# Performance work log

Measured on AMD Instinct MI355X. Metric: run time of the kernel, lower is better.

The kernel has to match this reference:

```python
import jax, jax.numpy as jnp
import numpy as np

VOCAB_SIZE = 62  # string.ascii_letters + string.digits
HIDDEN = 1024
STATE = int(HIDDEN * 4.0)  # state_size_mult=4.0
B, L = 2, 2048


def setup_inputs() -> dict:
    key = jax.random.key(0)
    ks = jax.random.split(key, 6)
    g = lambda k, shape, scale: (jax.random.normal(k, shape, jnp.float32) * scale)
    return {
        "tokens": jax.random.randint(ks[0], (B, L), 0, VOCAB_SIZE),
        "embed_w": g(ks[1], (VOCAB_SIZE, HIDDEN), 1.0),
        "norm_w": jnp.ones((HIDDEN,), jnp.float32),
        "in_w": g(ks[2], (HIDDEN, 4 * STATE), HIDDEN ** -0.5),
        "in_b": jnp.zeros((4 * STATE,), jnp.float32),
        "out_w": g(ks[3], (STATE, HIDDEN), STATE ** -0.5),
        "out_b": jnp.zeros((HIDDEN,), jnp.float32),
        "head_w": g(ks[4], (HIDDEN, VOCAB_SIZE), HIDDEN ** -0.5),
        "head_b": jnp.zeros((VOCAB_SIZE,), jnp.float32),
    }


def _rmsnorm(x, w, eps=1e-6):
    var = jnp.mean(x * x, axis=-1, keepdims=True)
    return x * jax.lax.rsqrt(var + eps) * w


def reference(tokens, embed_w, norm_w, in_w, in_b, out_w, out_b, head_w, head_b):
    # embedding lookup: [B, L, H]
    x = embed_w[tokens]
    res = x
    xn = _rmsnorm(x, norm_w)
    # single fused projection to (x_inner, a, b, c), each [B, L, STATE]
    proj = xn @ in_w + in_b
    xg, a_l, b_l, c_l = jnp.split(proj, 4, axis=-1)
    a = jax.nn.sigmoid(a_l)            # forget gate in (0,1)
    bx = jax.nn.sigmoid(b_l) * xg      # input contribution b_t * x_t
    # linear recurrence h_t = a_t * h_{t-1} + b_t * x_t via associative scan
    def comb(e1, e2):
        a1, h1 = e1
        a2, h2 = e2
        return a1 * a2, a2 * h1 + h2
    _, h = jax.lax.associative_scan(comb, (a, bx), axis=1)
    y = jax.nn.sigmoid(c_l) * h        # output gate c_t * h_t
    out = y @ out_w + out_b + res      # project back to hidden + residual
    return out @ head_w + head_b       # vocab logits [B, L, 62]
```

## Files before the change

### kernel.cpp

```cpp
#include <hip/hip_runtime.h>
#include <math.h>

#define HID   1024
#define STT   4096
#define MTOK  4096
#define LSEQ  2048
#define NCHUNK 64
#define CHUNK  32
#define VOCAB  62

typedef __attribute__((ext_vector_type(8))) short short8v;
typedef __attribute__((ext_vector_type(4))) float float4v;

typedef const __attribute__((address_space(1))) void* gptr_t;
typedef __attribute__((address_space(3))) void* lptr_t;

__device__ __forceinline__ float sigmoidf_(float x) {
    return 1.0f / (1.0f + __expf(-x));
}
__device__ __forceinline__ unsigned short f2bf(float f) {
    unsigned int u = __float_as_uint(f);
    unsigned int r = (u + 0x7fffu + ((u >> 16) & 1u)) >> 16;
    return (unsigned short)r;
}
__device__ __forceinline__ float bf2f(unsigned short b) {
    return __uint_as_float(((unsigned int)b) << 16);
}

__global__ __launch_bounds__(256) void fused_pre(
    const int* __restrict__ tokens, const float* __restrict__ embed_w,
    const float* __restrict__ norm_w, const float* __restrict__ in_w,
    const float* __restrict__ out_w, const float* __restrict__ head_w,
    const float* __restrict__ out_b, const float* __restrict__ head_b,
    unsigned short* __restrict__ in_wT, unsigned short* __restrict__ xn,
    unsigned short* __restrict__ W2T, float* __restrict__ E_head)
{
    __shared__ float sh[1056];
    int bid = blockIdx.x;
    int tid = threadIdx.x;
    if (bid < 16384) {
        float (*tile)[33] = (float (*)[33])sh;
        int c0 = (bid & 511) * 32, r0 = (bid >> 9) * 32;
        int r = tid >> 3, c4 = (tid & 7) << 2;
        float4 v = *(const float4*)(in_w + (size_t)(r0 + r) * 16384 + c0 + c4);
        tile[r][c4 + 0] = v.x; tile[r][c4 + 1] = v.y;
        tile[r][c4 + 2] = v.z; tile[r][c4 + 3] = v.w;
        __syncthreads();
        int oc = tid >> 3;
        int orr = (tid & 7) << 2;
        ushort4 o;
        o.x = f2bf(tile[orr + 0][oc]); o.y = f2bf(tile[orr + 1][oc]);
        o.z = f2bf(tile[orr + 2][oc]); o.w = f2bf(tile[orr + 3][oc]);
        *(ushort4*)(in_wT + (size_t)(c0 + oc) * 1024 + r0 + orr) = o;
    } else if (bid < 20480) {
        int m = bid - 16384;
        int tok = tokens[m];
        float4 x = ((const float4*)(embed_w + (size_t)tok * HID))[tid];
        float ss = x.x * x.x + x.y * x.y + x.z * x.z + x.w * x.w;
        for (int off = 32; off > 0; off >>= 1) ss += __shfl_down(ss, off);
        if ((tid & 63) == 0) sh[tid >> 6] = ss;
        __syncthreads();
        float tot = sh[0] + sh[1] + sh[2] + sh[3];
        float scale = rsqrtf(tot / (float)HID + 1e-6f);
        float4 w4 = ((const float4*)norm_w)[tid];
        ushort4 o;
        o.x = f2bf(x.x * scale * w4.x); o.y = f2bf(x.y * scale * w4.y);
        o.z = f2bf(x.z * scale * w4.z); o.w = f2bf(x.w * scale * w4.w);
        *(ushort4*)(xn + (size_t)m * HID + (tid << 2)) = o;
    } else if (bid < 21504) {
        float (*red)[4][64] = (float (*)[4][64])sh;
        int jc = tid >> 6, n = tid & 63;
        bool act = n < VOCAB;
        int k0 = (bid - 20480) * 4;
        float a[4] = {0.f, 0.f, 0.f, 0.f};
        int j0 = jc * 256;
        const float* w0 = out_w + (size_t)(k0 + 0) * HID;
        const float* w1 = out_w + (size_t)(k0 + 1) * HID;
        const float* w2 = out_w + (size_t)(k0 + 2) * HID;
        const float* w3 = out_w + (size_t)(k0 + 3) * HID;
        #pragma unroll 4
        for (int j = j0; j < j0 + 256; j++) {
            float h = act ? head_w[(size_t)j * VOCAB + n] : 0.f;
            a[0] = fmaf(w0[j], h, a[0]);
            a[1] = fmaf(w1[j], h, a[1]);
            a[2] = fmaf(w2[j], h, a[2]);
            a[3] = fmaf(w3[j], h, a[3]);
        }
        #pragma unroll
        for (int i = 0; i < 4; i++) red[jc][i][n] = a[i];
        __syncthreads();
        if (jc == 0) {
            #pragma unroll
            for (int i = 0; i < 4; i++) {
                float s = red[0][i][n] + red[1][i][n] + red[2][i][n] + red[3][i][n];
                W2T[(size_t)n * STT + k0 + i] = f2bf(s);
            }
        }
    } else {
        float (*red)[4][64] = (float (*)[4][64])sh;
        int jc = tid >> 6, n = tid & 63;
        bool act = n < VOCAB;
        int t = bid - 21504;
        const float* src = (t < VOCAB) ? (embed_w + (size_t)t * HID) : out_b;
        float acc = 0.f;
        if (act) {
            int j0 = jc * 256;
            #pragma unroll 4
            for (int j = j0; j < j0 + 256; j++)
                acc = fmaf(src[j], head_w[(size_t)j * VOCAB + n], acc);
        }
        red[jc][0][n] = acc;
        __syncthreads();
        if (tid < 64) {
            float s = red[0][0][n] + red[1][0][n] + red[2][0][n] + red[3][0][n];
            if (t == VOCAB && act) s += head_b[n];
            E_head[t * 64 + n] = s;
        }
    }
}

__global__ __launch_bounds__(512, 2) void gemm_in_mfma(
    const unsigned short* __restrict__ A, const unsigned short* __restrict__ B,
    const float* __restrict__ bias,
    unsigned short* __restrict__ a_out, unsigned short* __restrict__ bx_out,
    unsigned short* __restrict__ c_out,
    float* __restrict__ chunkA, float* __restrict__ chunkH)
{
    extern __shared__ unsigned short lds[];
    int tid = threadIdx.x;
    int wid = tid >> 6, lane = tid & 63;
    int wg = blockIdx.x;
    int xcd = wg & 7, loc = wg >> 3;
    int by = ((xcd >> 1) << 2) + (loc & 3);
    int bx = ((xcd & 1) << 5) + (loc >> 2);
    int m0 = by * 256, s0 = bx * 64;
    int wm = wid >> 2, wn = wid & 3;
    int lr = lane & 15, lk = lane >> 4;

    int cb0 = wid * 64, cb1 = 512 + wid * 64;
    int p0 = cb0 + lane, p1 = cb1 + lane;
    int row0 = p0 >> 2, ks0 = (p0 & 3) ^ ((row0 >> 1) & 3);
    int row1 = p1 >> 2, ks1 = (p1 & 3) ^ ((row1 >> 1) & 3);
    int arow0 = m0 + row0, arow1 = m0 + row1;
    int brow0 = ((row0 >> 6) << 12) + s0 + (row0 & 63);
    int brow1 = ((row1 >> 6) << 12) + s0 + (row1 & 63);

#define SHALF(grow0, grow1, b, which, kt, kk) do {                               \
    unsigned short* _d = lds + (b) * 32768 + (which) * 16384 + (kk) * 8192;      \
    __builtin_amdgcn_global_load_lds(                                            \
        (gptr_t)(const void*)(((which) ? B : A) + (size_t)(grow0) * 1024 +       \
                              (kt) * 64 + (kk) * 32 + ks0 * 8),                  \
        (lptr_t)(void*)(_d + (size_t)cb0 * 8), 16, 0, 0);                        \
    __builtin_amdgcn_global_load_lds(                                            \
        (gptr_t)(const void*)(((which) ? B : A) + (size_t)(grow1) * 1024 +       \
                              (kt) * 64 + (kk) * 32 + ks1 * 8),                  \
        (lptr_t)(void*)(_d + (size_t)cb1 * 8), 16, 0, 0);                        \
} while (0)

    int ksw = lk ^ ((lr >> 1) & 3);

#define RD_A(b, kk, mf) \
    (*(const short8v*)&lds[(b) * 32768 + (kk) * 8192 + \
        (((wm * 128 + (mf) * 16 + lr) << 2) + ksw) * 8])
#define RD_B(b, kk, nf) \
    (*(const short8v*)&lds[(b) * 32768 + 16384 + (kk) * 8192 + \
        ((((nf) * 64 + wn * 16 + lr) << 2) + ksw) * 8])

#define MFMA8x2(AF, B0, B1, n0i, n1i) do {                                       \
    __builtin_amdgcn_s_setprio(1);                                               \
    _Pragma("unroll")                                                            \
    for (int mf = 0; mf < 8; mf++) {                                             \
        acc[mf][n0i] = __builtin_amdgcn_mfma_f32_16x16x32_bf16(                  \
            (AF)[mf], (B0), acc[mf][n0i], 0, 0, 0);                              \
        acc[mf][n1i] = __builtin_amdgcn_mfma_f32_16x16x32_bf16(                  \
            (AF)[mf], (B1), acc[mf][n1i], 0, 0, 0);                              \
    }                                                                            \
    __builtin_amdgcn_s_setprio(0);                                               \
} while (0)

#define BAR_IN()  do { __builtin_amdgcn_s_barrier();                              \
    asm volatile("s_waitcnt lgkmcnt(0)" ::: "memory");                           \
    __builtin_amdgcn_sched_barrier(0); } while (0)
#define BAR_OUT() do { asm volatile("" ::: "memory");                             \
    __builtin_amdgcn_s_barrier(); } while (0)

    float4v acc[8][4];
    float4v z = {0.f, 0.f, 0.f, 0.f};
    #pragma unroll
    for (int i = 0; i < 8; i++)
        #pragma unroll
        for (int j = 0; j < 4; j++) acc[i][j] = z;

    SHALF(arow0, arow1, 0, 0, 0, 0); SHALF(brow0, brow1, 0, 1, 0, 0);
    SHALF(arow0, arow1, 0, 0, 0, 1); SHALF(brow0, brow1, 0, 1, 0, 1);
    asm volatile("s_waitcnt vmcnt(0)" ::: "memory");
    __builtin_amdgcn_s_barrier();

    short8v af[8], bf0, bf1;

    for (int kt = 0; kt < 16; ++kt) {
        int cur = kt & 1, nxt = cur ^ 1;
        int ktn = kt < 15 ? kt + 1 : 15;
        #pragma unroll
        for (int mf = 0; mf < 8; mf++) af[mf] = RD_A(cur, 0, mf);
        bf0 = RD_B(cur, 0, 0); bf1 = RD_B(cur, 0, 1);
        asm volatile("s_waitcnt vmcnt(4)" ::: "memory");
        SHALF(arow0, arow1, nxt, 0, ktn, 0);
        BAR_IN();
        MFMA8x2(af, bf0, bf1, 0, 1);
        BAR_OUT();
        bf0 = RD_B(cur, 0, 2); bf1 = RD_B(cur, 0, 3);
        SHALF(brow0, brow1, nxt, 1, ktn, 0);
        BAR_IN();
        MFMA8x2(af, bf0, bf1, 2, 3);
        BAR_OUT();
        #pragma unroll
        for (int mf = 0; mf < 8; mf++) af[mf] = RD_A(cur, 1, mf);
        bf0 = RD_B(cur, 1, 0); bf1 = RD_B(cur, 1, 1);
        asm volatile("s_waitcnt vmcnt(4)" ::: "memory");
        SHALF(arow0, arow1, nxt, 0, ktn, 1);
        BAR_IN();
        MFMA8x2(af, bf0, bf1, 0, 1);
        BAR_OUT();
        bf0 = RD_B(cur, 1, 2); bf1 = RD_B(cur, 1, 3);
        SHALF(brow0, brow1, nxt, 1, ktn, 1);
        BAR_IN();
        MFMA8x2(af, bf0, bf1, 2, 3);
        BAR_OUT();
    }

    int s = s0 + wn * 16 + lr;
    float b_xg = bias[s];
    float b_a  = bias[4096 + s];
    float b_b  = bias[8192 + s];
    float b_c  = bias[12288 + s];
    int rbase = lk << 2;
    int bb = m0 >> 11;
    int t0 = m0 & 2047;
    int ch = bb * STT + s;

    #pragma unroll
    for (int cc = 0; cc < 4; cc++) {
        float Afr[2], Hfr[2];
        #pragma unroll
        for (int e = 0; e < 2; e++) {
            int mf = cc * 2 + e;
            float Al = 1.f, Hl = 0.f;
            #pragma unroll
            for (int q = 0; q < 4; q++) {
                int m = m0 + wm * 128 + mf * 16 + rbase + q;
                size_t idx = (size_t)m * STT + s;
                float xg = acc[mf][0][q] + b_xg;
                float av = sigmoidf_(acc[mf][1][q] + b_a);
                float bxv = sigmoidf_(acc[mf][2][q] + b_b) * xg;
                float cv = sigmoidf_(acc[mf][3][q] + b_c);
                unsigned short au = f2bf(av), bu = f2bf(bxv);
                a_out[idx]  = au;
                bx_out[idx] = bu;
                c_out[idx]  = f2bf(cv);
                float ar = bf2f(au), br = bf2f(bu);
                Hl = fmaf(ar, Hl, br);
                Al = ar * Al;
            }
            #pragma unroll
            for (int d = 1; d <= 2; d <<= 1) {
                float Ap = __shfl(Al, lane - (d << 4));
                float Hp = __shfl(Hl, lane - (d << 4));
                if (lk >= d) { Hl = fmaf(Al, Hp, Hl); Al = Al * Ap; }
            }
            Afr[e] = Al; Hfr[e] = Hl;
        }
        if (lk == 3) {
            float Ac = Afr[1] * Afr[0];
            float Hc = fmaf(Afr[1], Hfr[0], Hfr[1]);
            int qg = (t0 >> 5) + wm * 4 + cc;
            chunkA[ch * NCHUNK + qg] = Ac;
            chunkH[ch * NCHUNK + qg] = Hc;
        }
    }
#undef SHALF
#undef RD_A
#undef RD_B
#undef MFMA8x2
#undef BAR_IN
#undef BAR_OUT
}

__global__ __launch_bounds__(256) void scan_phase2(
    const float* __restrict__ chunkA, const float* __restrict__ chunkH,
    float* __restrict__ carry)
{
    int ch = blockIdx.x * 256 + threadIdx.x;
    float c = 0.f;
    for (int q = 0; q < NCHUNK; q++) {
        carry[ch * NCHUNK + q] = c;
        c = fmaf(chunkA[ch * NCHUNK + q], c, chunkH[ch * NCHUNK + q]);
    }
}

__global__ __launch_bounds__(256) void scan_logits(
    const unsigned short* __restrict__ a_buf, const unsigned short* __restrict__ bx_buf,
    const unsigned short* __restrict__ c_buf, const float* __restrict__ carry,
    const unsigned short* __restrict__ W2T, float* __restrict__ part)
{
    __shared__ __align__(16) unsigned short y_lds[128 * 128];
    __shared__ __align__(16) unsigned short b_lds[64 * 128];
    int tid = threadIdx.x;
    int wg = blockIdx.x;
    int mt = wg & 31, sl = wg >> 5;
    int m0 = mt * 128;
    int bb = m0 >> 11;
    int q0 = (m0 & 2047) >> 5;
    int lane = tid & 63, wid = tid >> 6;
    int lr = lane & 15, lk = lane >> 4;

    float4v acc[2][4];
    float4v z = {0.f, 0.f, 0.f, 0.f};
    #pragma unroll
    for (int e = 0; e < 2; e++)
        #pragma unroll
        for (int nf = 0; nf < 4; nf++) acc[e][nf] = z;

    for (int ks = 0; ks < 4; ++ks) {
        int sbase = sl * 512 + ks * 128;
        #pragma unroll
        for (int i = 0; i < 4; i++) {
            int cb = i * 256 + wid * 64;
            int p = cb + lane;
            int row = p >> 4, csw = p & 15;
            int c = csw ^ (row & 7);
            __builtin_amdgcn_global_load_lds(
                (gptr_t)(const void*)(W2T + (size_t)row * STT + sbase + c * 8),
                (lptr_t)(void*)(b_lds + (size_t)cb * 8), 16, 0, 0);
        }
        {
            int chq = wid;
            int s = sbase + lane * 2;
            int q = q0 + chq;
            size_t cidx = ((size_t)(bb * STT + s)) * NCHUNK + q;
            float h0 = carry[cidx];
            float h1 = carry[cidx + NCHUNK];
            size_t gb = (size_t)(m0 + chq * 32) * STT + s;
            const unsigned int* ap = (const unsigned int*)(a_buf + gb);
            const unsigned int* bp = (const unsigned int*)(bx_buf + gb);
            const unsigned int* cp = (const unsigned int*)(c_buf + gb);
            const int stride = STT / 2;
            #pragma unroll 4
            for (int i = 0; i < 32; i++) {
                unsigned int au = ap[(size_t)i * stride];
                unsigned int bu = bp[(size_t)i * stride];
                unsigned int cu = cp[(size_t)i * stride];
                float a0 = bf2f((unsigned short)(au & 0xffff));
                float a1 = bf2f((unsigned short)(au >> 16));
                float b0 = bf2f((unsigned short)(bu & 0xffff));
                float b1 = bf2f((unsigned short)(bu >> 16));
                float c0 = bf2f((unsigned short)(cu & 0xffff));
                float c1 = bf2f((unsigned short)(cu >> 16));
                h0 = fmaf(a0, h0, b0);
                h1 = fmaf(a1, h1, b1);
                unsigned int yp = (unsigned int)f2bf(c0 * h0) |
                                  ((unsigned int)f2bf(c1 * h1) << 16);
                int row = chq * 32 + i;
                int cw = (lane >> 2) ^ (row & 7);
                *(unsigned int*)&y_lds[row * 128 + (cw << 3) + (lane & 3) * 2] = yp;
            }
        }
        __syncthreads();
        #pragma unroll
        for (int kt2 = 0; kt2 < 4; kt2++) {
            short8v af[2], bf[4];
            #pragma unroll
            for (int e = 0; e < 2; e++) {
                int row = (wid * 2 + e) * 16 + lr;
                int c = kt2 * 4 + lk;
                af[e] = *(const short8v*)&y_lds[row * 128 + ((c ^ (row & 7)) << 3)];
            }
            #pragma unroll
            for (int nf = 0; nf < 4; nf++) {
                int row = nf * 16 + lr;
                int c = kt2 * 4 + lk;
                bf[nf] = *(const short8v*)&b_lds[row * 128 + ((c ^ (row & 7)) << 3)];
            }
            __builtin_amdgcn_s_setprio(1);
            #pragma unroll
            for (int e = 0; e < 2; e++)
                #pragma unroll
                for (int nf = 0; nf < 4; nf++)
                    acc[e][nf] = __builtin_amdgcn_mfma_f32_16x16x32_bf16(
                        af[e], bf[nf], acc[e][nf], 0, 0, 0);
            __builtin_amdgcn_s_setprio(0);
        }
        __syncthreads();
    }

    float* pb = part + (size_t)sl * MTOK * 64;
    int rbase = lk << 2;
    #pragma unroll
    for (int e = 0; e < 2; e++)
        #pragma unroll
        for (int nf = 0; nf < 4; nf++) {
            int n = nf * 16 + lr;
            #pragma unroll
            for (int q = 0; q < 4; q++) {
                int m = m0 + (wid * 2 + e) * 16 + rbase + q;
                pb[(size_t)m * 64 + n] = acc[e][nf][q];
            }
        }
}

__global__ __launch_bounds__(64) void logits_reduce(
    const float* __restrict__ part, const float* __restrict__ E_head,
    const int* __restrict__ tokens, float* __restrict__ logits)
{
    int m = blockIdx.x;
    int n = threadIdx.x;
    if (n >= VOCAB) return;
    int tok = tokens[m];
    float s = E_head[tok * 64 + n] + E_head[VOCAB * 64 + n];
    #pragma unroll
    for (int sl = 0; sl < 8; sl++)
        s += part[(size_t)sl * MTOK * 64 + (size_t)m * 64 + n];
    logits[(size_t)m * VOCAB + n] = s;
}

extern "C" void kernel_launch(void* const* d_in, const int* in_sizes, int n_in,
                              void* d_out, int out_size, void* d_ws, size_t ws_size,
                              hipStream_t stream) {
    const int*   tokens  = (const int*)d_in[0];
    const float* embed_w = (const float*)d_in[1];
    const float* norm_w  = (const float*)d_in[2];
    const float* in_w    = (const float*)d_in[3];
    const float* in_b    = (const float*)d_in[4];
    const float* out_w   = (const float*)d_in[5];
    const float* out_b   = (const float*)d_in[6];
    const float* head_w  = (const float*)d_in[7];
    const float* head_b  = (const float*)d_in[8];
    float* logits = (float*)d_out;

    char* w = (char*)d_ws;
    unsigned short* a_buf  = (unsigned short*)w;
    unsigned short* bx_buf = (unsigned short*)(w + 33554432);
    unsigned short* c_buf  = (unsigned short*)(w + 67108864);
    unsigned short* W2T    = (unsigned short*)(w + 100663296);
    float*          E_head = (float*)(w + 101711872);
    float*          part   = (float*)(w + 102760448);
    unsigned short* in_wT  = (unsigned short*)(w + 167772160);
    unsigned short* xn     = (unsigned short*)(w + 201326592);
    float* chunkA = (float*)(w + 209715200);
    float* chunkH = chunkA + 8192 * NCHUNK;
    float* carry  = chunkH + 8192 * NCHUNK;

    hipLaunchKernelGGL(fused_pre, dim3(16384 + 4096 + 1024 + VOCAB + 1), dim3(256), 0, stream,
                       tokens, embed_w, norm_w, in_w, out_w, head_w, out_b, head_b,
                       in_wT, xn, W2T, E_head);
    hipLaunchKernelGGL(gemm_in_mfma, dim3(1024), dim3(512), 131072, stream,
                       xn, in_wT, in_b, a_buf, bx_buf, c_buf, chunkA, chunkH);
    hipLaunchKernelGGL(scan_phase2, dim3(32), dim3(256), 0, stream,
                       chunkA, chunkH, carry);
    hipLaunchKernelGGL(scan_logits, dim3(256), dim3(256), 0, stream,
                       a_buf, bx_buf, c_buf, carry, W2T, part);
    hipLaunchKernelGGL(logits_reduce, dim3(MTOK), dim3(64), 0, stream,
                       part, E_head, tokens, logits);
}
```

Before: 265.2 us.

## Replace partial-sum buffer and reduce kernel with atomic logits accumulation

Removes the logits_reduce kernel and the partial buffer. A new scan2_init kernel runs the carry scan and also writes the bias/embedding-head base logits. scan_logits now splits the state dimension into 16 slices over 512 blocks and atomically adds its partial results straight into the logits. This saves a launch and the partial-buffer round trip, and doubles the scan_logits grid, at the cost of float atomics contention and non-deterministic summation order.

```diff
diff --git a/kernel.cpp b/kernel.cpp
--- a/kernel.cpp
+++ b/kernel.cpp
@@ -286,22 +286,35 @@
 #undef BAR_OUT
 }
 
-__global__ __launch_bounds__(256) void scan_phase2(
+__global__ __launch_bounds__(256) void scan2_init(
     const float* __restrict__ chunkA, const float* __restrict__ chunkH,
-    float* __restrict__ carry)
+    const float* __restrict__ E_head, const int* __restrict__ tokens,
+    float* __restrict__ carry, float* __restrict__ logits)
 {
-    int ch = blockIdx.x * 256 + threadIdx.x;
-    float c = 0.f;
-    for (int q = 0; q < NCHUNK; q++) {
-        carry[ch * NCHUNK + q] = c;
-        c = fmaf(chunkA[ch * NCHUNK + q], c, chunkH[ch * NCHUNK + q]);
+    int bid = blockIdx.x;
+    int tid = threadIdx.x;
+    if (bid < 32) {
+        int ch = bid * 256 + tid;
+        float c = 0.f;
+        for (int q = 0; q < NCHUNK; q++) {
+            carry[ch * NCHUNK + q] = c;
+            c = fmaf(chunkA[ch * NCHUNK + q], c, chunkH[ch * NCHUNK + q]);
+        }
+    } else {
+        int m = (bid - 32) * 4 + (tid >> 6);
+        int n = tid & 63;
+        if (n < VOCAB) {
+            int tok = tokens[m];
+            logits[(size_t)m * VOCAB + n] =
+                E_head[tok * 64 + n] + E_head[VOCAB * 64 + n];
+        }
     }
 }
 
 __global__ __launch_bounds__(256) void scan_logits(
     const unsigned short* __restrict__ a_buf, const unsigned short* __restrict__ bx_buf,
     const unsigned short* __restrict__ c_buf, const float* __restrict__ carry,
-    const unsigned short* __restrict__ W2T, float* __restrict__ part)
+    const unsigned short* __restrict__ W2T, float* __restrict__ logits)
 {
     __shared__ __align__(16) unsigned short y_lds[128 * 128];
     __shared__ __align__(16) unsigned short b_lds[64 * 128];
@@ -321,8 +334,8 @@
         #pragma unroll
         for (int nf = 0; nf < 4; nf++) acc[e][nf] = z;
 
-    for (int ks = 0; ks < 4; ++ks) {
-        int sbase = sl * 512 + ks * 128;
+    for (int ks = 0; ks < 2; ++ks) {
+        int sbase = sl * 256 + ks * 128;
         #pragma unroll
         for (int i = 0; i < 4; i++) {
             int cb = i * 256 + wid * 64;
@@ -393,34 +406,20 @@
         __syncthreads();
     }
 
-    float* pb = part + (size_t)sl * MTOK * 64;
     int rbase = lk << 2;
     #pragma unroll
     for (int e = 0; e < 2; e++)
         #pragma unroll
         for (int nf = 0; nf < 4; nf++) {
             int n = nf * 16 + lr;
-            #pragma unroll
-            for (int q = 0; q < 4; q++) {
-                int m = m0 + (wid * 2 + e) * 16 + rbase + q;
-                pb[(size_t)m * 64 + n] = acc[e][nf][q];
-            }
-        }
-}
-
-__global__ __launch_bounds__(64) void logits_reduce(
-    const float* __restrict__ part, const float* __restrict__ E_head,
-    const int* __restrict__ tokens, float* __restrict__ logits)
-{
-    int m = blockIdx.x;
-    int n = threadIdx.x;
-    if (n >= VOCAB) return;
-    int tok = tokens[m];
-    float s = E_head[tok * 64 + n] + E_head[VOCAB * 64 + n];
-    #pragma unroll
-    for (int sl = 0; sl < 8; sl++)
-        s += part[(size_t)sl * MTOK * 64 + (size_t)m * 64 + n];
-    logits[(size_t)m * VOCAB + n] = s;
+            if (n < VOCAB) {
+                #pragma unroll
+                for (int q = 0; q < 4; q++) {
+                    int m = m0 + (wid * 2 + e) * 16 + rbase + q;
+                    atomicAdd(&logits[(size_t)m * VOCAB + n], acc[e][nf][q]);
+                }
+            }
+        }
 }
 
 extern "C" void kernel_launch(void* const* d_in, const int* in_sizes, int n_in,
@@ -443,7 +442,6 @@
     unsigned short* c_buf  = (unsigned short*)(w + 67108864);
     unsigned short* W2T    = (unsigned short*)(w + 100663296);
     float*          E_head = (float*)(w + 101711872);
-    float*          part   = (float*)(w + 102760448);
     unsigned short* in_wT  = (unsigned short*)(w + 167772160);
     unsigned short* xn     = (unsigned short*)(w + 201326592);
     float* chunkA = (float*)(w + 209715200);
@@ -455,10 +453,8 @@
                        in_wT, xn, W2T, E_head);
     hipLaunchKernelGGL(gemm_in_mfma, dim3(1024), dim3(512), 131072, stream,
                        xn, in_wT, in_b, a_buf, bx_buf, c_buf, chunkA, chunkH);
-    hipLaunchKernelGGL(scan_phase2, dim3(32), dim3(256), 0, stream,
-                       chunkA, chunkH, carry);
-    hipLaunchKernelGGL(scan_logits, dim3(256), dim3(256), 0, stream,
-                       a_buf, bx_buf, c_buf, carry, W2T, part);
-    hipLaunchKernelGGL(logits_reduce, dim3(MTOK), dim3(64), 0, stream,
-                       part, E_head, tokens, logits);
-}
+    hipLaunchKernelGGL(scan2_init, dim3(32 + 1024), dim3(256), 0, stream,
+                       chunkA, chunkH, E_head, tokens, carry, logits);
+    hipLaunchKernelGGL(scan_logits, dim3(512), dim3(256), 0, stream,
+                       a_buf, bx_buf, c_buf, carry, W2T, logits);
+}
```

After: 277.4 us. 1.05x slower.

## Simplify input GEMM to K=32 double-buffered stages with single barrier pair

Applied to the files above, without the earlier changes.

Replaces the finely interleaved K=64 pipeline, which had four half-stage loads and barrier pairs per iteration, with a simple double-buffered loop over K=32 tiles. Each iteration issues one stage load, waits, runs a single barrier, and does all 32 MFMAs. LDS use halves from 128KB to 64KB, which could allow two workgroups per CU. The cost is that far less data is in flight per K step, so memory latency is hidden less well, and there are twice as many iterations, each with barrier overhead.

```diff
diff --git a/kernel.cpp b/kernel.cpp
--- a/kernel.cpp
+++ b/kernel.cpp
@@ -145,44 +145,31 @@
     int brow0 = ((row0 >> 6) << 12) + s0 + (row0 & 63);
     int brow1 = ((row1 >> 6) << 12) + s0 + (row1 & 63);
 
-#define SHALF(grow0, grow1, b, which, kt, kk) do {                               \
-    unsigned short* _d = lds + (b) * 32768 + (which) * 16384 + (kk) * 8192;      \
+#define STAGE(b, kt) do {                                                        \
+    unsigned short* _a = lds + (b) * 16384;                                      \
+    unsigned short* _b = _a + 8192;                                              \
     __builtin_amdgcn_global_load_lds(                                            \
-        (gptr_t)(const void*)(((which) ? B : A) + (size_t)(grow0) * 1024 +       \
-                              (kt) * 64 + (kk) * 32 + ks0 * 8),                  \
-        (lptr_t)(void*)(_d + (size_t)cb0 * 8), 16, 0, 0);                        \
+        (gptr_t)(const void*)(A + (size_t)arow0 * 1024 + (kt) * 32 + ks0 * 8),   \
+        (lptr_t)(void*)(_a + (size_t)cb0 * 8), 16, 0, 0);                        \
     __builtin_amdgcn_global_load_lds(                                            \
-        (gptr_t)(const void*)(((which) ? B : A) + (size_t)(grow1) * 1024 +       \
-                              (kt) * 64 + (kk) * 32 + ks1 * 8),                  \
-        (lptr_t)(void*)(_d + (size_t)cb1 * 8), 16, 0, 0);                        \
+        (gptr_t)(const void*)(A + (size_t)arow1 * 1024 + (kt) * 32 + ks1 * 8),   \
+        (lptr_t)(void*)(_a + (size_t)cb1 * 8), 16, 0, 0);                        \
+    __builtin_amdgcn_global_load_lds(                                            \
+        (gptr_t)(const void*)(B + (size_t)brow0 * 1024 + (kt) * 32 + ks0 * 8),   \
+        (lptr_t)(void*)(_b + (size_t)cb0 * 8), 16, 0, 0);                        \
+    __builtin_amdgcn_global_load_lds(                                            \
+        (gptr_t)(const void*)(B + (size_t)brow1 * 1024 + (kt) * 32 + ks1 * 8),   \
+        (lptr_t)(void*)(_b + (size_t)cb1 * 8), 16, 0, 0);                        \
 } while (0)
 
     int ksw = lk ^ ((lr >> 1) & 3);
 
-#define RD_A(b, kk, mf) \
-    (*(const short8v*)&lds[(b) * 32768 + (kk) * 8192 + \
+#define RD_A(b, mf) \
+    (*(const short8v*)&lds[(b) * 16384 + \
         (((wm * 128 + (mf) * 16 + lr) << 2) + ksw) * 8])
-#define RD_B(b, kk, nf) \
-    (*(const short8v*)&lds[(b) * 32768 + 16384 + (kk) * 8192 + \
+#define RD_B(b, nf) \
+    (*(const short8v*)&lds[(b) * 16384 + 8192 + \
         ((((nf) * 64 + wn * 16 + lr) << 2) + ksw) * 8])
-
-#define MFMA8x2(AF, B0, B1, n0i, n1i) do {                                       \
-    __builtin_amdgcn_s_setprio(1);                                               \
-    _Pragma("unroll")                                                            \
-    for (int mf = 0; mf < 8; mf++) {                                             \
-        acc[mf][n0i] = __builtin_amdgcn_mfma_f32_16x16x32_bf16(                  \
-            (AF)[mf], (B0), acc[mf][n0i], 0, 0, 0);                              \
-        acc[mf][n1i] = __builtin_amdgcn_mfma_f32_16x16x32_bf16(                  \
-            (AF)[mf], (B1), acc[mf][n1i], 0, 0, 0);                              \
-    }                                                                            \
-    __builtin_amdgcn_s_setprio(0);                                               \
-} while (0)
-
-#define BAR_IN()  do { __builtin_amdgcn_s_barrier();                              \
-    asm volatile("s_waitcnt lgkmcnt(0)" ::: "memory");                           \
-    __builtin_amdgcn_sched_barrier(0); } while (0)
-#define BAR_OUT() do { asm volatile("" ::: "memory");                             \
-    __builtin_amdgcn_s_barrier(); } while (0)
 
     float4v acc[8][4];
     float4v z = {0.f, 0.f, 0.f, 0.f};
@@ -191,42 +178,33 @@
         #pragma unroll
         for (int j = 0; j < 4; j++) acc[i][j] = z;
 
-    SHALF(arow0, arow1, 0, 0, 0, 0); SHALF(brow0, brow1, 0, 1, 0, 0);
-    SHALF(arow0, arow1, 0, 0, 0, 1); SHALF(brow0, brow1, 0, 1, 0, 1);
-    asm volatile("s_waitcnt vmcnt(0)" ::: "memory");
-    __builtin_amdgcn_s_barrier();
-
-    short8v af[8], bf0, bf1;
-
-    for (int kt = 0; kt < 16; ++kt) {
+    STAGE(0, 0);
+
+    for (int kt = 0; kt < 32; ++kt) {
         int cur = kt & 1, nxt = cur ^ 1;
-        int ktn = kt < 15 ? kt + 1 : 15;
-        #pragma unroll
-        for (int mf = 0; mf < 8; mf++) af[mf] = RD_A(cur, 0, mf);
-        bf0 = RD_B(cur, 0, 0); bf1 = RD_B(cur, 0, 1);
-        asm volatile("s_waitcnt vmcnt(4)" ::: "memory");
-        SHALF(arow0, arow1, nxt, 0, ktn, 0);
-        BAR_IN();
-        MFMA8x2(af, bf0, bf1, 0, 1);
-        BAR_OUT();
-        bf0 = RD_B(cur, 0, 2); bf1 = RD_B(cur, 0, 3);
-        SHALF(brow0, brow1, nxt, 1, ktn, 0);
-        BAR_IN();
-        MFMA8x2(af, bf0, bf1, 2, 3);
-        BAR_OUT();
-        #pragma unroll
-        for (int mf = 0; mf < 8; mf++) af[mf] = RD_A(cur, 1, mf);
-        bf0 = RD_B(cur, 1, 0); bf1 = RD_B(cur, 1, 1);
-        asm volatile("s_waitcnt vmcnt(4)" ::: "memory");
-        SHALF(arow0, arow1, nxt, 0, ktn, 1);
-        BAR_IN();
-        MFMA8x2(af, bf0, bf1, 0, 1);
-        BAR_OUT();
-        bf0 = RD_B(cur, 1, 2); bf1 = RD_B(cur, 1, 3);
-        SHALF(brow0, brow1, nxt, 1, ktn, 1);
-        BAR_IN();
-        MFMA8x2(af, bf0, bf1, 2, 3);
-        BAR_OUT();
+        if (kt < 31) {
+            STAGE(nxt, kt + 1);
+            asm volatile("s_waitcnt vmcnt(4)" ::: "memory");
+        } else {
+            asm volatile("s_waitcnt vmcnt(0)" ::: "memory");
+        }
+        __builtin_amdgcn_s_barrier();
+        asm volatile("" ::: "memory");
+        short8v af[8], bf[4];
+        #pragma unroll
+        for (int mf = 0; mf < 8; mf++) af[mf] = RD_A(cur, mf);
+        #pragma unroll
+        for (int nf = 0; nf < 4; nf++) bf[nf] = RD_B(cur, nf);
+        __builtin_amdgcn_s_setprio(1);
+        #pragma unroll
+        for (int mf = 0; mf < 8; mf++)
+            #pragma unroll
+            for (int nf = 0; nf < 4; nf++)
+                acc[mf][nf] = __builtin_amdgcn_mfma_f32_16x16x32_bf16(
+                    af[mf], bf[nf], acc[mf][nf], 0, 0, 0);
+        __builtin_amdgcn_s_setprio(0);
+        asm volatile("" ::: "memory");
+        __builtin_amdgcn_s_barrier();
     }
 
     int s = s0 + wn * 16 + lr;
@@ -278,12 +256,9 @@
             chunkH[ch * NCHUNK + qg] = Hc;
         }
     }
-#undef SHALF
+#undef STAGE
 #undef RD_A
 #undef RD_B
-#undef MFMA8x2
-#undef BAR_IN
-#undef BAR_OUT
 }
 
 __global__ __launch_bounds__(256) void scan_phase2(
@@ -453,7 +428,7 @@
     hipLaunchKernelGGL(fused_pre, dim3(16384 + 4096 + 1024 + VOCAB + 1), dim3(256), 0, stream,
                        tokens, embed_w, norm_w, in_w, out_w, head_w, out_b, head_b,
                        in_wT, xn, W2T, E_head);
-    hipLaunchKernelGGL(gemm_in_mfma, dim3(1024), dim3(512), 131072, stream,
+    hipLaunchKernelGGL(gemm_in_mfma, dim3(1024), dim3(512), 65536, stream,
                        xn, in_wT, in_b, a_buf, bx_buf, c_buf, chunkA, chunkH);
     hipLaunchKernelGGL(scan_phase2, dim3(32), dim3(256), 0, stream,
                        chunkA, chunkH, carry);
```

New measurement: 269.4 us. No clear change (+1.6%).
